# Kernel optimization log

Measured on AMD Instinct MI355X. Metric: run time of the kernel, lower is better.

## Reference

```python
import jax, jax.numpy as jnp
import numpy as np

B, C, T, Fd = 4, 256, 64, 256
H = 8
HID = int(C * 2.0)
LN_EPS = 1e-5
L2_EPS = 1e-12


def _layernorm(x, g, b):
    mu = jnp.mean(x, axis=-1, keepdims=True)
    var = jnp.mean((x - mu) ** 2, axis=-1, keepdims=True)
    return (x - mu) * jax.lax.rsqrt(var + LN_EPS) * g + b


def _l2norm(x):
    n = jnp.sqrt(jnp.sum(x * x, axis=-1, keepdims=True))
    return x / jnp.maximum(n, L2_EPS)


def setup_inputs() -> dict:
    key = jax.random.key(0)
    ks = jax.random.split(key, 8)
    s = 0.02
    return {
        "x": jax.random.normal(ks[0], (B, C, T, Fd), dtype=jnp.float32),
        "norm1_g": jnp.ones((C,), jnp.float32),
        "norm1_b": jnp.zeros((C,), jnp.float32),
        "Wqkv": jax.random.normal(ks[1], (C, 3 * C), jnp.float32) * s,
        "dw_w": jax.random.normal(ks[2], (3 * C, 1, 3), jnp.float32) * s,  # depthwise conv1d kernel (O, I/g=1, K)
        "Wproj": jax.random.normal(ks[3], (C, C), jnp.float32) * s,
        "temperature": jnp.full((H, 1, 1), 0.5, jnp.float32),
        "norm2_g": jnp.ones((C,), jnp.float32),
        "norm2_b": jnp.zeros((C,), jnp.float32),
        "W1": jax.random.normal(ks[4], (C, HID), jnp.float32) * s,
        "b1": jnp.zeros((HID,), jnp.float32),
        "W2": jax.random.normal(ks[5], (HID, C), jnp.float32) * s,
        "b2": jnp.zeros((C,), jnp.float32),
    }


def reference(x, norm1_g, norm1_b, Wqkv, dw_w, Wproj, temperature,
              norm2_g, norm2_b, W1, b1, W2, b2):
    b, c, t, f = x.shape
    # axis='freq': (b c t f) -> ((b t) f c)
    xs = jnp.transpose(x, (0, 2, 3, 1)).reshape(b * t, f, c)

    xn = _layernorm(xs, norm1_g, norm1_b)
    qkv = xn @ Wqkv                                  # (bt, f, 3c)
    # depthwise conv1d along the sequence (freq) axis, kernel 3, pad 1
    qkv = jnp.transpose(qkv, (0, 2, 1))              # (bt, 3c, f)
    qkv = jax.lax.conv_general_dilated(
        qkv, dw_w, window_strides=(1,), padding=[(1, 1)],
        feature_group_count=3 * c,
        dimension_numbers=("NCH", "OIH", "NCH"))
    qkv = jnp.transpose(qkv, (0, 2, 1))              # (bt, f, 3c)

    q, k, v = jnp.split(qkv, 3, axis=-1)
    d = c // H
    def heads(z):  # (bt, s, c) -> (bt, h, s, d)
        return jnp.transpose(z.reshape(b * t, f, H, d), (0, 2, 1, 3))
    q, k, v = heads(q), heads(k), heads(v)

    q = _l2norm(q)
    k = _l2norm(k)
    attn = jnp.einsum("bhsd,bhtd->bhst", q, k) * temperature  # temp broadcasts (h,1,1)
    attn = jax.nn.softmax(attn, axis=-1)
    out = jnp.einsum("bhst,bhtd->bhsd", attn, v)
    out = jnp.transpose(out, (0, 2, 1, 3)).reshape(b * t, f, c)
    out = out @ Wproj
    out = out + xs

    h = _layernorm(out, norm2_g, norm2_b)
    h = jax.nn.gelu(h @ W1 + b1, approximate=False) @ W2 + b2
    out = out + h

    # ((b t) f c) -> (b c t f)
    out = out.reshape(b, t, f, c)
    return jnp.transpose(out, (0, 3, 1, 2))
```

## Files before the change

kernel.cpp:

```cpp
#include <hip/hip_runtime.h>
#include <math.h>

#define Bv 4
#define Cv 256
#define Tv 64
#define Fv 256
#define Hv 8
#define HIDv 512
#define Mv 65536
#define CTF (Cv * Tv * Fv)
#define TF (Tv * Fv)

typedef unsigned short u16;
typedef __attribute__((ext_vector_type(8))) short bfx8;
typedef __attribute__((ext_vector_type(4))) float f32x4;

__device__ __forceinline__ float bf2f(u16 u) {
  return __uint_as_float(((unsigned int)u) << 16);
}
__device__ __forceinline__ u16 f2bf(float f) {
  unsigned int x = __float_as_uint(f);
  unsigned int r = x + 0x7fffu + ((x >> 16) & 1u);
  return (u16)(r >> 16);
}
__device__ __forceinline__ unsigned int cvtpk(float a, float b) {
  unsigned int r;
  asm("v_cvt_pk_bf16_f32 %0, %1, %2" : "=v"(r) : "v"(a), "v"(b));
  return r;
}

__launch_bounds__(256)
__global__ void transpose_w(const float* __restrict__ in, u16* __restrict__ out,
                            int K, int N) {
  __shared__ float t[32][33];
  const int n0 = blockIdx.x * 32, k0 = blockIdx.y * 32;
  const int c = threadIdx.x & 31, r = threadIdx.x >> 5;
#pragma unroll
  for (int i = 0; i < 4; ++i)
    t[r + 8 * i][c] = in[(size_t)(k0 + r + 8 * i) * N + n0 + c];
  __syncthreads();
#pragma unroll
  for (int i = 0; i < 4; ++i)
    out[(size_t)(n0 + r + 8 * i) * K + k0 + c] = f2bf(t[c][r + 8 * i]);
}

__launch_bounds__(256)
__global__ void ln1_kernel(const float* __restrict__ x, const float* __restrict__ g,
                           const float* __restrict__ bta, u16* __restrict__ xn) {
  __shared__ float tile[256][33];
  __shared__ float red1[8][32];
  __shared__ float red2[8][32];
  __shared__ float mu_s[32];
  __shared__ float rs_s[32];
  const int tid = threadIdx.x;
  const int blk = blockIdx.x;
  const int n = blk >> 3;
  const int f0 = (blk & 7) << 5;
  const int bb = n >> 6, tt = n & 63;
  const float* xb = x + (size_t)bb * CTF + (size_t)tt * Fv;
  const int fl = tid & 31, c0 = tid >> 5;
#pragma unroll
  for (int i = 0; i < 32; ++i) {
    int c = i * 8 + c0;
    tile[c][fl] = xb[(size_t)c * TF + f0 + fl];
  }
  __syncthreads();
  const int col = tid & 31, part = tid >> 5;
  float s = 0.f, s2 = 0.f;
#pragma unroll
  for (int i = 0; i < 32; ++i) {
    float v = tile[part * 32 + i][col];
    s += v; s2 += v * v;
  }
  red1[part][col] = s; red2[part][col] = s2;
  __syncthreads();
  if (tid < 32) {
    float S1 = 0.f, S2 = 0.f;
#pragma unroll
    for (int p = 0; p < 8; ++p) { S1 += red1[p][tid]; S2 += red2[p][tid]; }
    float m = S1 * (1.f / 256.f);
    float var = S2 * (1.f / 256.f) - m * m;
    mu_s[tid] = m;
    rs_s[tid] = rsqrtf(var + 1e-5f);
  }
  __syncthreads();
  const float gv = g[tid], bv = bta[tid];
  u16* ob = xn + ((size_t)n * 256 + f0) * 256 + tid;
#pragma unroll
  for (int fl2 = 0; fl2 < 32; ++fl2) {
    ob[(size_t)fl2 * 256] = f2bf((tile[tid][fl2] - mu_s[fl2]) * rs_s[fl2] * gv + bv);
  }
}

template <int K, int N, int EPI>
__launch_bounds__(256)
__global__ void gemm_mfma(const u16* __restrict__ A, const u16* __restrict__ Bt,
                          void* __restrict__ Cc, const float* __restrict__ aux0,
                          const u16* __restrict__ aux1) {
  constexpr int LDSTR = 88;
  __shared__ u16 As[128 * LDSTR];
  __shared__ u16 Bs[128 * LDSTR];
  const int tid = threadIdx.x;
  const int lane = tid & 63, wid = tid >> 6;
  const int m0 = blockIdx.y * 128, n0 = blockIdx.x * 128;
  const int wm = (wid & 1) * 64, wn = (wid >> 1) * 64;
  const int lm = lane & 15, quad = lane >> 4;

  const int srow = tid >> 3, sch = tid & 7;

  f32x4 acc[4][4] = {};
  for (int k0 = 0; k0 < K; k0 += 64) {
    bfx8 ar[4], br[4];
#pragma unroll
    for (int i = 0; i < 4; ++i) {
      const int row = srow + i * 32;
      ar[i] = *(const bfx8*)(A + (size_t)(m0 + row) * K + k0 + sch * 8);
      br[i] = *(const bfx8*)(Bt + (size_t)(n0 + row) * K + k0 + sch * 8);
    }
    __syncthreads();
#pragma unroll
    for (int i = 0; i < 4; ++i) {
      const int row = srow + i * 32;
      *(bfx8*)&As[row * LDSTR + sch * 8] = ar[i];
      *(bfx8*)&Bs[row * LDSTR + sch * 8] = br[i];
    }
    __syncthreads();
#pragma unroll
    for (int s = 0; s < 2; ++s) {
      bfx8 af[4], bf[4];
#pragma unroll
      for (int t = 0; t < 4; ++t) {
        af[t] = *(const bfx8*)&As[(wm + t * 16 + lm) * LDSTR + s * 32 + quad * 8];
        bf[t] = *(const bfx8*)&Bs[(wn + t * 16 + lm) * LDSTR + s * 32 + quad * 8];
      }
#pragma unroll
      for (int tm = 0; tm < 4; ++tm)
#pragma unroll
        for (int tn = 0; tn < 4; ++tn)
          acc[tm][tn] = __builtin_amdgcn_mfma_f32_16x16x32_bf16(af[tm], bf[tn], acc[tm][tn], 0, 0, 0);
    }
  }

  const int row_l = quad * 4;
  const int nn = m0 >> 8;
  const int bb = nn >> 6, tt = nn & 63;
  const int srow_base = (m0 & 255) + wm;
  float bcol[4];
  if constexpr (EPI == 2 || EPI == 3) {
#pragma unroll
    for (int tn = 0; tn < 4; ++tn) bcol[tn] = aux0[n0 + wn + tn * 16 + lm];
  }
#pragma unroll
  for (int tm = 0; tm < 4; ++tm) {
    const int grow0 = m0 + wm + tm * 16 + row_l;
    const int sr0 = srow_base + tm * 16 + row_l;
#pragma unroll
    for (int tn = 0; tn < 4; ++tn) {
      const int gcol = n0 + wn + tn * 16 + lm;
      if constexpr (EPI == 0) {
#pragma unroll
        for (int r = 0; r < 4; ++r)
          ((u16*)Cc)[(size_t)(grow0 + r) * N + gcol] = f2bf(acc[tm][tn][r]);
      } else if constexpr (EPI == 1) {
        const float4 xv = *(const float4*)(aux0 + (size_t)bb * CTF + (size_t)gcol * TF + tt * Fv + sr0);
        const float xr[4] = {xv.x, xv.y, xv.z, xv.w};
#pragma unroll
        for (int r = 0; r < 4; ++r)
          ((u16*)Cc)[(size_t)(grow0 + r) * N + gcol] = f2bf(acc[tm][tn][r] + xr[r]);
      } else if constexpr (EPI == 2) {
#pragma unroll
        for (int r = 0; r < 4; ++r) {
          float v = acc[tm][tn][r] + bcol[tn];
          float y = 0.79788456080286536f * (v + 0.044715f * v * v * v);
          float th = 1.f - 2.f / (__expf(2.f * y) + 1.f);
          ((u16*)Cc)[(size_t)(grow0 + r) * N + gcol] = f2bf(0.5f * v * (1.f + th));
        }
      } else {
        float4 o;
#pragma unroll
        for (int r = 0; r < 4; ++r) {
          float res = bf2f(aux1[(size_t)(grow0 + r) * 256 + gcol]);
          ((float*)&o)[r] = acc[tm][tn][r] + bcol[tn] + res;
        }
        *(float4*)((float*)Cc + (size_t)bb * CTF + (size_t)gcol * TF + tt * Fv + sr0) = o;
      }
    }
  }
}

__launch_bounds__(512)
__global__ void attn_kernel(const u16* __restrict__ qkv, const float* __restrict__ dw,
                            const float* __restrict__ temp, u16* __restrict__ attn_out) {
  __shared__ u16 Kc[2][64 * 40];
  __shared__ u16 Vt[2][32 * 72];
  __shared__ float l_s[256];
  const int tid = threadIdx.x;
  const int lane = tid & 63, w = tid >> 6;
  const int l15 = lane & 15, quad = lane >> 4;
  const int n = blockIdx.x >> 3, h = blockIdx.x & 7;
  const int h32 = h * 32;
  const u16* base = qkv + (size_t)n * 256 * 768;
  const float th2 = temp[h] * 1.44269504089f;

  bfx8 bq[2];
  {
    const int d0q = quad * 8;
    float wq[3][8];
#pragma unroll
    for (int j = 0; j < 8; ++j)
#pragma unroll
      for (int t = 0; t < 3; ++t) wq[t][j] = dw[(h32 + d0q + j) * 3 + t];
#pragma unroll
    for (int ct = 0; ct < 2; ++ct) {
      const int row = w * 32 + ct * 16 + l15;
      const u16* src = base + (size_t)row * 768 + h32 + d0q;
      float v[8];
      const bfx8 bm = *(const bfx8*)src;
#pragma unroll
      for (int j = 0; j < 8; ++j) v[j] = wq[1][j] * bf2f((u16)bm[j]);
      if (row > 0) {
        const bfx8 bp = *(const bfx8*)(src - 768);
#pragma unroll
        for (int j = 0; j < 8; ++j) v[j] += wq[0][j] * bf2f((u16)bp[j]);
      }
      if (row < 255) {
        const bfx8 bn = *(const bfx8*)(src + 768);
#pragma unroll
        for (int j = 0; j < 8; ++j) v[j] += wq[2][j] * bf2f((u16)bn[j]);
      }
      float ssq = 0.f;
#pragma unroll
      for (int j = 0; j < 8; ++j) ssq += v[j] * v[j];
      ssq += __shfl_xor(ssq, 16);
      ssq += __shfl_xor(ssq, 32);
      const float inv = 1.f / fmaxf(sqrtf(ssq), 1e-12f);
      union { unsigned int u[4]; bfx8 b; } qb;
#pragma unroll
      for (int m = 0; m < 4; ++m) qb.u[m] = cvtpk(v[2 * m] * inv, v[2 * m + 1] * inv);
      bq[ct] = qb.b;
    }
  }

  const bool isK = tid < 256;
  const int sV = tid & 255;
  const int krow = sV >> 2, kd0 = (sV & 3) * 8;
  const int vd = sV & 31, vko = sV >> 5;
  float wu[24];
  if (isK) {
#pragma unroll
    for (int j = 0; j < 8; ++j)
#pragma unroll
      for (int t = 0; t < 3; ++t) wu[t * 8 + j] = dw[(256 + h32 + kd0 + j) * 3 + t];
  } else {
#pragma unroll
    for (int t = 0; t < 3; ++t) wu[t] = dw[(512 + h32 + vd) * 3 + t];
  }

  bfx8 km = {}, kp = {}, kn = {};
  u16 xs[10];

  auto stage_load = [&](int c) {
    if (isK) {
      const int gr = c * 64 + krow;
      const u16* src = base + (size_t)gr * 768 + 256 + h32 + kd0;
      km = *(const bfx8*)src;
      kp = (gr > 0) ? *(const bfx8*)(src - 768) : bfx8{};
      kn = (gr < 255) ? *(const bfx8*)(src + 768) : bfx8{};
    } else {
      const int g0 = c * 64 + vko * 8;
      const u16* src = base + (size_t)g0 * 768 + 512 + h32 + vd;
#pragma unroll
      for (int k = 0; k < 10; ++k) {
        const int gr = g0 + k - 1;
        xs[k] = (gr >= 0 && gr < 256) ? src[(ptrdiff_t)(k - 1) * 768] : (u16)0;
      }
    }
  };
  auto stage_finish = [&](int b) {
    if (isK) {
      float v[8];
#pragma unroll
      for (int j = 0; j < 8; ++j)
        v[j] = wu[8 + j] * bf2f((u16)km[j]) + wu[j] * bf2f((u16)kp[j]) +
               wu[16 + j] * bf2f((u16)kn[j]);
      float ssq = 0.f;
#pragma unroll
      for (int j = 0; j < 8; ++j) ssq += v[j] * v[j];
      ssq += __shfl_xor(ssq, 1);
      ssq += __shfl_xor(ssq, 2);
      const float inv = 1.f / fmaxf(sqrtf(ssq), 1e-12f);
      union { unsigned int u[4]; bfx8 b; } kb;
#pragma unroll
      for (int m = 0; m < 4; ++m) kb.u[m] = cvtpk(v[2 * m] * inv, v[2 * m + 1] * inv);
      *(bfx8*)&Kc[b][krow * 40 + kd0] = kb.b;
    } else {
      float x[10];
#pragma unroll
      for (int k = 0; k < 10; ++k) x[k] = bf2f(xs[k]);
      union { unsigned int u[4]; bfx8 b; } ob;
#pragma unroll
      for (int m = 0; m < 4; ++m) {
        float a0 = wu[0] * x[2 * m] + wu[1] * x[2 * m + 1] + wu[2] * x[2 * m + 2];
        float a1 = wu[0] * x[2 * m + 1] + wu[1] * x[2 * m + 2] + wu[2] * x[2 * m + 3];
        ob.u[m] = cvtpk(a0, a1);
      }
      const int po = vko ^ ((vd >> 3) & 3);
      *(bfx8*)&Vt[b][vd * 72 + po * 8] = ob.b;
    }
  };

  f32x4 acc[2][2] = {};
  float lsum[2] = {0.f, 0.f};
  const f32x4 zf = {0.f, 0.f, 0.f, 0.f};
  const int fo = (l15 >> 3) & 1;

  stage_load(0);
  stage_finish(0);
  __syncthreads();

  for (int c = 0; c < 4; ++c) {
    const int b = c & 1;
    if (c < 3) stage_load(c + 1);

    bfx8 af[4];
#pragma unroll
    for (int rt = 0; rt < 4; ++rt)
      af[rt] = *(const bfx8*)&Kc[b][(rt * 16 + l15) * 40 + quad * 8];
#pragma unroll
    for (int ct = 0; ct < 2; ++ct) {
      unsigned int pu[4], pv[4];
#pragma unroll
      for (int rt = 0; rt < 4; ++rt) {
        f32x4 sc = __builtin_amdgcn_mfma_f32_16x16x32_bf16(af[rt], bq[ct], zf, 0, 0, 0);
        float e0 = exp2f(sc[0] * th2), e1 = exp2f(sc[1] * th2);
        float e2 = exp2f(sc[2] * th2), e3 = exp2f(sc[3] * th2);
        lsum[ct] += (e0 + e1) + (e2 + e3);
        pu[rt] = cvtpk(e0, e1);
        pv[rt] = cvtpk(e2, e3);
      }
#pragma unroll
      for (int ks = 0; ks < 2; ++ks) {
        auto su = __builtin_amdgcn_permlane32_swap(pu[2 * ks], pu[2 * ks + 1], false, false);
        auto tu = __builtin_amdgcn_permlane16_swap(su[0], su[1], false, false);
        auto sv = __builtin_amdgcn_permlane32_swap(pv[2 * ks], pv[2 * ks + 1], false, false);
        auto tv = __builtin_amdgcn_permlane16_swap(sv[0], sv[1], false, false);
        union { unsigned int u[4]; bfx8 b; } ap;
        ap.u[0] = tu[0]; ap.u[1] = tv[0]; ap.u[2] = tu[1]; ap.u[3] = tv[1];
        const bfx8 bv0 = *(const bfx8*)&Vt[b][l15 * 72 + (ks * 4 + (quad ^ fo)) * 8];
        const bfx8 bv1 = *(const bfx8*)&Vt[b][(16 + l15) * 72 + (ks * 4 + (quad ^ (2 | fo))) * 8];
        acc[ct][0] = __builtin_amdgcn_mfma_f32_16x16x32_bf16(ap.b, bv0, acc[ct][0], 0, 0, 0);
        acc[ct][1] = __builtin_amdgcn_mfma_f32_16x16x32_bf16(ap.b, bv1, acc[ct][1], 0, 0, 0);
      }
    }
    if (c < 3) stage_finish(b ^ 1);
    __syncthreads();
  }

#pragma unroll
  for (int ct = 0; ct < 2; ++ct) {
    float L = lsum[ct];
    L += __shfl_xor(L, 16);
    L += __shfl_xor(L, 32);
    if (quad == 0) l_s[w * 32 + ct * 16 + l15] = L;
  }
#pragma unroll
  for (int ct = 0; ct < 2; ++ct) {
    const f32x4 l4 = *(const f32x4*)&l_s[w * 32 + ct * 16 + quad * 4];
    float rinv[4];
#pragma unroll
    for (int r = 0; r < 4; ++r) rinv[r] = 1.f / l4[r];
#pragma unroll
    for (int dh = 0; dh < 2; ++dh)
#pragma unroll
      for (int r = 0; r < 4; ++r) {
        const int qrow = w * 32 + ct * 16 + quad * 4 + r;
        attn_out[((size_t)n * 256 + qrow) * 256 + h32 + dh * 16 + l15] =
            f2bf(acc[ct][dh][r] * rinv[r]);
      }
  }
}

__launch_bounds__(256)
__global__ void ln2_kernel(const u16* __restrict__ in, const float* __restrict__ g,
                           const float* __restrict__ bta, u16* __restrict__ out) {
  const int lane = threadIdx.x & 63;
  const size_t row = (size_t)blockIdx.x * 4 + (threadIdx.x >> 6);
  const ushort4 u = ((const ushort4*)(in + row * 256))[lane];
  const float vx = bf2f(u.x), vy = bf2f(u.y), vz = bf2f(u.z), vw = bf2f(u.w);
  float s = vx + vy + vz + vw;
  float s2 = vx * vx + vy * vy + vz * vz + vw * vw;
#pragma unroll
  for (int m = 32; m >= 1; m >>= 1) {
    s += __shfl_xor(s, m, 64);
    s2 += __shfl_xor(s2, m, 64);
  }
  const float mu = s * (1.f / 256.f);
  const float rs = rsqrtf(s2 * (1.f / 256.f) - mu * mu + 1e-5f);
  const float4 gv = ((const float4*)g)[lane];
  const float4 bv = ((const float4*)bta)[lane];
  ushort4 o;
  o.x = f2bf((vx - mu) * rs * gv.x + bv.x);
  o.y = f2bf((vy - mu) * rs * gv.y + bv.y);
  o.z = f2bf((vz - mu) * rs * gv.z + bv.z);
  o.w = f2bf((vw - mu) * rs * gv.w + bv.w);
  ((ushort4*)(out + row * 256))[lane] = o;
}

extern "C" void kernel_launch(void* const* d_in, const int* in_sizes, int n_in,
                              void* d_out, int out_size, void* d_ws, size_t ws_size,
                              hipStream_t stream) {
  const float* x     = (const float*)d_in[0];
  const float* n1g   = (const float*)d_in[1];
  const float* n1b   = (const float*)d_in[2];
  const float* Wqkv  = (const float*)d_in[3];
  const float* dw    = (const float*)d_in[4];
  const float* Wproj = (const float*)d_in[5];
  const float* temp  = (const float*)d_in[6];
  const float* n2g   = (const float*)d_in[7];
  const float* n2b   = (const float*)d_in[8];
  const float* W1    = (const float*)d_in[9];
  const float* b1    = (const float*)d_in[10];
  const float* W2    = (const float*)d_in[11];
  const float* b2    = (const float*)d_in[12];

  char* ws = (char*)d_ws;
  u16* xn       = (u16*)(ws);
  u16* qkv      = (u16*)(ws + (32ull << 20));
  u16* attn_out = xn;
  u16* out1     = (u16*)(ws + (32ull << 20));
  u16* xn2      = xn;
  u16* h1       = (u16*)(ws + (64ull << 20));
  u16* w2t      = xn;

  char* ob = (char*)d_out;
  u16* wqkvt  = (u16*)(ob);
  u16* wprojt = (u16*)(ob + (1ull << 20));
  u16* w1t    = (u16*)(ob + 1572864ull);

  transpose_w<<<dim3(24, 8), 256, 0, stream>>>(Wqkv, wqkvt, 256, 768);
  transpose_w<<<dim3(8, 8), 256, 0, stream>>>(Wproj, wprojt, 256, 256);
  transpose_w<<<dim3(16, 8), 256, 0, stream>>>(W1, w1t, 256, 512);

  ln1_kernel<<<2048, 256, 0, stream>>>(x, n1g, n1b, xn);
  gemm_mfma<256, 768, 0><<<dim3(6, 512), 256, 0, stream>>>(xn, wqkvt, qkv, nullptr, nullptr);
  attn_kernel<<<2048, 512, 0, stream>>>(qkv, dw, temp, attn_out);
  gemm_mfma<256, 256, 1><<<dim3(2, 512), 256, 0, stream>>>(attn_out, wprojt, out1, x, nullptr);
  ln2_kernel<<<16384, 256, 0, stream>>>(out1, n2g, n2b, xn2);
  gemm_mfma<256, 512, 2><<<dim3(4, 512), 256, 0, stream>>>(xn2, W1 ? w1t : w1t, h1, b1, nullptr);
  transpose_w<<<dim3(8, 16), 256, 0, stream>>>(W2, w2t, 512, 256);
  gemm_mfma<512, 256, 3><<<dim3(2, 512), 256, 0, stream>>>(h1, w2t, d_out, b2, out1);
}
```

Measured before the change: 416.0 us.

## Use direct global-to-LDS loads with XOR swizzle and remapped block order in GEMM

The GEMM tile loads now go straight from global memory into LDS with global_load_lds instead of passing through registers. LDS padding is replaced by an XOR swizzle on 16-byte chunks so fragment reads avoid bank conflicts. Block IDs are remapped across groups of eight, which looks aimed at spreading neighbouring tiles across XCDs or improving cache locality. This reduces register pressure and VALU store work, but loads are still issued synchronously with no double buffering, and correctness depends on the per-lane LDS layout matching what global_load_lds writes.

```diff
diff --git a/kernel.cpp b/kernel.cpp
--- a/kernel.cpp
+++ b/kernel.cpp
@@ -97,32 +97,34 @@
 __global__ void gemm_mfma(const u16* __restrict__ A, const u16* __restrict__ Bt,
                           void* __restrict__ Cc, const float* __restrict__ aux0,
                           const u16* __restrict__ aux1) {
-  constexpr int LDSTR = 88;
-  __shared__ u16 As[128 * LDSTR];
-  __shared__ u16 Bs[128 * LDSTR];
+  constexpr int GX = N / 128;
+  __shared__ u16 As[128 * 64];
+  __shared__ u16 Bs[128 * 64];
   const int tid = threadIdx.x;
   const int lane = tid & 63, wid = tid >> 6;
-  const int m0 = blockIdx.y * 128, n0 = blockIdx.x * 128;
+  int id = blockIdx.y * GX + blockIdx.x;
+  const int qch = (GX * gridDim.y) >> 3;
+  id = (id & 7) * qch + (id >> 3);
+  const int m0 = (id / GX) * 128, n0 = (id % GX) * 128;
   const int wm = (wid & 1) * 64, wn = (wid >> 1) * 64;
   const int lm = lane & 15, quad = lane >> 4;
 
-  const int srow = tid >> 3, sch = tid & 7;
+  const int l8 = lane >> 3, c8 = lane & 7;
+  const int gc = (c8 ^ l8) * 8;
 
   f32x4 acc[4][4] = {};
   for (int k0 = 0; k0 < K; k0 += 64) {
-    bfx8 ar[4], br[4];
+    __syncthreads();
 #pragma unroll
     for (int i = 0; i < 4; ++i) {
-      const int row = srow + i * 32;
-      ar[i] = *(const bfx8*)(A + (size_t)(m0 + row) * K + k0 + sch * 8);
-      br[i] = *(const bfx8*)(Bt + (size_t)(n0 + row) * K + k0 + sch * 8);
-    }
-    __syncthreads();
-#pragma unroll
-    for (int i = 0; i < 4; ++i) {
-      const int row = srow + i * 32;
-      *(bfx8*)&As[row * LDSTR + sch * 8] = ar[i];
-      *(bfx8*)&Bs[row * LDSTR + sch * 8] = br[i];
+      const int rb = wid * 32 + i * 8;
+      const int row = rb + l8;
+      __builtin_amdgcn_global_load_lds(
+          (const __attribute__((address_space(1))) void*)(A + (size_t)(m0 + row) * K + k0 + gc),
+          (__attribute__((address_space(3))) void*)(&As[rb * 64]), 16, 0, 0);
+      __builtin_amdgcn_global_load_lds(
+          (const __attribute__((address_space(1))) void*)(Bt + (size_t)(n0 + row) * K + k0 + gc),
+          (__attribute__((address_space(3))) void*)(&Bs[rb * 64]), 16, 0, 0);
     }
     __syncthreads();
 #pragma unroll
@@ -130,8 +132,10 @@
       bfx8 af[4], bf[4];
 #pragma unroll
       for (int t = 0; t < 4; ++t) {
-        af[t] = *(const bfx8*)&As[(wm + t * 16 + lm) * LDSTR + s * 32 + quad * 8];
-        bf[t] = *(const bfx8*)&Bs[(wn + t * 16 + lm) * LDSTR + s * 32 + quad * 8];
+        const int ra = wm + t * 16 + lm;
+        const int rbr = wn + t * 16 + lm;
+        af[t] = *(const bfx8*)&As[ra * 64 + (((s * 4 + quad) ^ (ra & 7))) * 8];
+        bf[t] = *(const bfx8*)&Bs[rbr * 64 + (((s * 4 + quad) ^ (rbr & 7))) * 8];
       }
 #pragma unroll
       for (int tm = 0; tm < 4; ++tm)
```

New measurement: 395.4 us. 1.05x faster.
